# Kernel tuning notes

Hardware: AMD Instinct MI355X
Metric: run time of the kernel (lower is better)

Reference implementation:

```python
import jax, jax.numpy as jnp
import numpy as np

BATCH, SEQ = 2, 2048
HID = 2048          # hidden_size
INTER = 4096        # intermediate_size
STATE = 16          # ssm_state_size
RANK = 128          # time_step_rank
K = 4               # conv_kernel


def setup_inputs() -> dict:
    key = jax.random.key(0)
    ks = jax.random.split(key, 8)
    s = 0.02
    return {
        "hidden_states": jax.random.normal(ks[0], (BATCH, SEQ, HID), jnp.float32),
        "in_proj_w": jax.random.normal(ks[1], (2 * INTER, HID), jnp.float32) * s,
        "conv_w": jax.random.normal(ks[2], (INTER, 1, K), jnp.float32) * s,   # depthwise (O, I/g=1, K)
        "conv_b": jnp.zeros((INTER,), jnp.float32),
        "x_proj_w": jax.random.normal(ks[3], (RANK + 2 * STATE, INTER), jnp.float32) * s,
        "dt_proj_w": jax.random.normal(ks[4], (INTER, RANK), jnp.float32) * s,
        "dt_proj_b": jax.random.normal(ks[5], (INTER,), jnp.float32) * s,
        "A_log": jnp.log(jnp.broadcast_to(jnp.arange(1, STATE + 1, dtype=jnp.float32), (INTER, STATE))),
        "D": jnp.ones((INTER,), jnp.float32),
        "out_proj_w": jax.random.normal(ks[6], (HID, INTER), jnp.float32) * s,
    }


def reference(hidden_states, in_proj_w, conv_w, conv_b, x_proj_w,
              dt_proj_w, dt_proj_b, A_log, D, out_proj_w):
    B, L, _ = hidden_states.shape
    # in_proj -> (B, L, 2*INTER), split into u (SSM input) and gate
    proj = jnp.einsum('blh,ph->blp', hidden_states, in_proj_w)
    u, gate = jnp.split(proj, 2, axis=-1)                       # (B, L, INTER) each
    # depthwise causal conv1d on channel-major layout (B, INTER, L)
    uc = jnp.swapaxes(u, 1, 2)
    conv = jax.lax.conv_general_dilated(
        uc, conv_w, window_strides=(1,), padding=[(K - 1, 0)],
        dimension_numbers=('NCH', 'OIH', 'NCH'), feature_group_count=INTER)
    u = jax.nn.silu(conv + conv_b[None, :, None])               # (B, INTER, L)
    # x_proj: dt-rank + B + C, computed in fp32 like the original
    ssm_p = jnp.einsum('bdl,pd->blp', u, x_proj_w).astype(jnp.float32)
    dt_r, Bm, Cm = jnp.split(ssm_p, [RANK, RANK + STATE], axis=-1)  # (B,L,RANK),(B,L,N),(B,L,N)
    dt = jax.nn.softplus(jnp.einsum('blr,dr->bld', dt_r, dt_proj_w) + dt_proj_b)  # (B, L, INTER)
    A = -jnp.exp(A_log)                                         # (INTER, STATE)

    def step(state, xs):
        dt_t, B_t, C_t, u_t = xs                                # (B,D),(B,N),(B,N),(B,D)
        dA = jnp.exp(dt_t[:, :, None] * A[None])                # (B, D, N)
        state = dA * state + (dt_t * u_t)[:, :, None] * B_t[:, None, :]
        y = jnp.einsum('bdn,bn->bd', state, C_t)
        return state, y

    xs = (jnp.swapaxes(dt, 0, 1),        # (L, B, D)
          jnp.swapaxes(Bm, 0, 1),        # (L, B, N)
          jnp.swapaxes(Cm, 0, 1),        # (L, B, N)
          jnp.moveaxis(u, 2, 0))         # (L, B, D)
    init = jnp.zeros((B, INTER, STATE), jnp.float32)
    _, ys = jax.lax.scan(step, init, xs)                        # (L, B, D)

    y = jnp.moveaxis(ys, 0, 1) + jnp.swapaxes(u, 1, 2) * D[None, None, :]  # skip connection
    y = y * jax.nn.silu(gate)
    return jnp.einsum('bld,hd->blh', y, out_proj_w)             # (B, L, HID)
```

## Files before the change

kernel.cpp:

```cpp
#include <hip/hip_runtime.h>

typedef unsigned int u32;
typedef unsigned short u16;
typedef float f32x4 __attribute__((ext_vector_type(4)));
typedef float f32x16 __attribute__((ext_vector_type(16)));
typedef u16 us4 __attribute__((ext_vector_type(4)));
typedef u16 us8 __attribute__((ext_vector_type(8)));
typedef __bf16 bf16x8 __attribute__((ext_vector_type(8)));

__device__ __forceinline__ u16 f2bf(float f) {
  u32 u = __builtin_bit_cast(u32, f);
  u += 0x7fffu + ((u >> 16) & 1u);
  return (u16)(u >> 16);
}
__device__ __forceinline__ float bf2f(u16 h) {
  u32 u = ((u32)h) << 16;
  return __builtin_bit_cast(float, u);
}
__device__ __forceinline__ void async16(const void* g, void* l) {
  __builtin_amdgcn_global_load_lds((const __attribute__((address_space(1))) void*)g,
                                   (__attribute__((address_space(3))) void*)l, 16, 0, 0);
}

#define STG(GP, LP, OFF, KOFF)                              \
  {                                                         \
    async16((GP) + (KOFF), (LP) + (OFF));                   \
    async16((GP) + 128L * K + (KOFF), (LP) + (OFF) + 4096); \
  }

#define PHASE4(SET, KS, STAGE_STMT, VMW_STMT)                           \
  {                                                                     \
    const u16* Ap_ = As + (SET) * 16384 + (KS) * 8192;                  \
    const u16* Bp_ = Bs + (SET) * 16384 + (KS) * 8192;                  \
    us8 af[8], bf[4];                                                   \
    _Pragma("unroll") for (int i = 0; i < 8; ++i)                       \
        af[i] = *(const us8*)(Ap_ + ra[i]);                             \
    _Pragma("unroll") for (int i = 0; i < 4; ++i)                       \
        bf[i] = *(const us8*)(Bp_ + rb[i]);                             \
    STAGE_STMT;                                                         \
    VMW_STMT;                                                           \
    __builtin_amdgcn_s_setprio(1);                                      \
    _Pragma("unroll") for (int nf = 0; nf < 4; ++nf)                    \
        _Pragma("unroll") for (int mf = 0; mf < 8; ++mf)                \
            acc[mf][nf] = __builtin_amdgcn_mfma_f32_16x16x32_bf16(      \
                __builtin_bit_cast(bf16x8, af[mf]),                     \
                __builtin_bit_cast(bf16x8, bf[nf]), acc[mf][nf],        \
                0, 0, 0);                                               \
    __builtin_amdgcn_s_setprio(0);                                      \
    __builtin_amdgcn_s_barrier();                                       \
  }

__global__ __launch_bounds__(512, 2) void gemm256(const u16* __restrict__ A,
                                                  const u16* __restrict__ B,
                                                  u16* __restrict__ U,
                                                  u16* __restrict__ G, int K) {
  __shared__ __align__(16) u16 As[32768];
  __shared__ __align__(16) u16 Bs[32768];
  const int tid = threadIdx.x;
  const int lane = tid & 63;
  const int wave = tid >> 6;
  const int wm = wave >> 2;
  const int wn = wave & 3;
  const int l15 = lane & 15;
  const int kc2 = lane >> 4;
  const int pc2s = kc2 ^ ((l15 >> 1) & 3);

  const int nbx = (int)gridDim.x;
  const int d = (int)blockIdx.y * nbx + (int)blockIdx.x;
  const int cpn = nbx >> 3;
  const int xcd = d & 7;
  const int s = d >> 3;
  const long colBase = (long)(xcd * cpn + (s % cpn)) << 8;
  const long rowBase = (long)(s / cpn) << 8;

  const int c0 = ((tid & 3) ^ ((tid >> 3) & 3)) << 3;
  const u16* Ag = A + (rowBase + (tid >> 2)) * (long)K + c0;
  const u16* Bg = B + (colBase + (tid >> 2)) * (long)K + c0;
  u16* Alds = As + tid * 8;
  u16* Blds = Bs + tid * 8;

  int ra[8], rb[4];
#pragma unroll
  for (int mf = 0; mf < 8; ++mf)
    ra[mf] = (wm * 128 + mf * 16 + l15) * 32 + pc2s * 8;
#pragma unroll
  for (int nf = 0; nf < 4; ++nf)
    rb[nf] = (wn * 64 + nf * 16 + l15) * 32 + pc2s * 8;

  f32x4 acc[8][4] = {};

  STG(Ag, Alds, 0, 0);
  STG(Bg, Blds, 0, 0);
  STG(Ag, Alds, 8192, 32);
  STG(Bg, Blds, 8192, 32);
  STG(Ag, Alds, 16384, 64);
  STG(Bg, Blds, 16384, 64);
  asm volatile("s_waitcnt vmcnt(8)" ::: "memory");
  __builtin_amdgcn_s_barrier();

  const int nIter = K >> 7;
  for (int t = 0; t < nIter; ++t) {
    const int k1 = (2 * t + 1) * 64;
    const int k2 = (2 * t + 2) * 64;
    const int k3 = (2 * t + 3) * 64;
    const bool full = (t < nIter - 1);
    PHASE4(0, 0,
           {
             STG(Ag, Alds, 24576, k1 + 32);
             STG(Bg, Blds, 24576, k1 + 32);
           },
           { asm volatile("s_waitcnt vmcnt(8)" ::: "memory"); });
    PHASE4(0, 1,
           {
             if (full) {
               STG(Ag, Alds, 0, k2);
               STG(Bg, Blds, 0, k2);
             }
           },
           {
             if (full) asm volatile("s_waitcnt vmcnt(8)" ::: "memory");
             else asm volatile("s_waitcnt vmcnt(4)" ::: "memory");
           });
    PHASE4(1, 0,
           {
             if (full) {
               STG(Ag, Alds, 8192, k2 + 32);
               STG(Bg, Blds, 8192, k2 + 32);
             }
           },
           {
             if (full) asm volatile("s_waitcnt vmcnt(8)" ::: "memory");
             else asm volatile("s_waitcnt vmcnt(0)" ::: "memory");
           });
    PHASE4(1, 1,
           {
             if (full) {
               STG(Ag, Alds, 16384, k3);
               STG(Bg, Blds, 16384, k3);
             }
           },
           { if (full) asm volatile("s_waitcnt vmcnt(8)" ::: "memory"); });
  }

  const int gate = (colBase >= 4096);
  u16* Out = gate ? G : U;
  const long cb = gate ? (colBase - 4096) : colBase;
#pragma unroll
  for (int mf = 0; mf < 8; ++mf) {
    long row0 = rowBase + wm * 128 + mf * 16 + (lane >> 4) * 4;
#pragma unroll
    for (int nf = 0; nf < 4; ++nf) {
      long col = cb + wn * 64 + nf * 16 + l15;
#pragma unroll
      for (int r = 0; r < 4; ++r) {
        float v = acc[mf][nf][r];
        if (gate) v = v / (1.f + __expf(-v));
        Out[(row0 + r) * 4096 + col] = f2bf(v);
      }
    }
  }
}

template <int ACT, bool SPLITK = false>
__global__ __launch_bounds__(256) void gemm_bt(const u16* __restrict__ A,
                                               const u16* __restrict__ B,
                                               void* __restrict__ Cv,
                                               const float* __restrict__ bias,
                                               int K, int ldc) {
  __shared__ __align__(16) u16 As[128 * 64];
  __shared__ __align__(16) u16 Bs[128 * 64];
  const int tid = threadIdx.x;
  const int lane = tid & 63;
  const int wave = tid >> 6;
  const int ln = lane & 31;
  const int hw = lane >> 5;
  const int wm = (wave >> 1) << 6;
  const int wn = (wave & 1) << 6;
  const long rowBase = (long)blockIdx.y << 7;
  const long colBase = (long)blockIdx.x << 7;

  int kStart = 0, kEnd = K;
  if constexpr (SPLITK) {
    int kn = K / gridDim.z;
    kStart = blockIdx.z * kn;
    kEnd = kStart + kn;
  }

  const int rr = tid >> 3;
  const int qg = (tid & 7) ^ (rr & 7);
  const u16* Ag = A + (rowBase + rr) * (long)K + qg * 8;
  const u16* Bg = B + (colBase + rr) * (long)K + qg * 8;
  u16* Al = As + tid * 8;
  u16* Bl = Bs + tid * 8;

  f32x16 acc[2][2] = {};
  const int l7 = ln & 7;

  for (int k0 = kStart; k0 < kEnd; k0 += 64) {
#pragma unroll
    for (int c = 0; c < 4; ++c) {
      async16(Ag + 32L * c * K + k0, Al + 2048 * c);
      async16(Bg + 32L * c * K + k0, Bl + 2048 * c);
    }
    __syncthreads();
#pragma unroll
    for (int s = 0; s < 4; ++s) {
      const int xa = ((s * 2 + hw) ^ l7) * 8;
      us8 af[2], bfr[2];
#pragma unroll
      for (int i = 0; i < 2; ++i)
        af[i] = *(const us8*)(As + (wm + i * 32 + ln) * 64 + xa);
#pragma unroll
      for (int i = 0; i < 2; ++i)
        bfr[i] = *(const us8*)(Bs + (wn + i * 32 + ln) * 64 + xa);
#pragma unroll
      for (int i = 0; i < 2; ++i)
#pragma unroll
        for (int j = 0; j < 2; ++j)
          acc[i][j] = __builtin_amdgcn_mfma_f32_32x32x16_bf16(
              __builtin_bit_cast(bf16x8, af[i]), __builtin_bit_cast(bf16x8, bfr[j]),
              acc[i][j], 0, 0, 0);
    }
    __syncthreads();
  }

  float* Cf = (float*)Cv;
  if constexpr (SPLITK)
    Cf += (size_t)blockIdx.z * ((size_t)gridDim.y * 128 * ldc);

#pragma unroll
  for (int i = 0; i < 2; ++i)
#pragma unroll
    for (int j = 0; j < 2; ++j)
#pragma unroll
      for (int r = 0; r < 16; ++r) {
        long row = rowBase + wm + i * 32 + (r & 3) + 8 * (r >> 2) + 4 * hw;
        long col = colBase + wn + j * 32 + ln;
        float v = acc[i][j][r];
        if constexpr (ACT == 0) {
          Cf[row * ldc + col] = v;
        } else if constexpr (ACT == 3) {
          v += bias[col];
          float sp = (v > 20.f) ? v : log1pf(__expf(v));
          Cf[row * ldc + col] = sp;
        } else if constexpr (ACT == 4) {
          v += bias[col];
          float sp = (v > 20.f) ? v : log1pf(__expf(v));
          ((u16*)Cv)[row * ldc + col] = f2bf(sp);
        }
      }
}

__device__ __forceinline__ void cvt8(const float* __restrict__ in,
                                     u16* __restrict__ out, int i) {
  f32x4 v0 = ((const f32x4*)in)[i * 2];
  f32x4 v1 = ((const f32x4*)in)[i * 2 + 1];
  us8 o;
  o[0] = f2bf(v0[0]); o[1] = f2bf(v0[1]); o[2] = f2bf(v0[2]); o[3] = f2bf(v0[3]);
  o[4] = f2bf(v1[0]); o[5] = f2bf(v1[1]); o[6] = f2bf(v1[2]); o[7] = f2bf(v1[3]);
  ((us8*)out)[i] = o;
}
__global__ __launch_bounds__(256) void cvt_all(
    const float* __restrict__ hs, const float* __restrict__ wIn,
    const float* __restrict__ wOut, const float* __restrict__ wDt,
    const float* __restrict__ wX, u16* __restrict__ Xb, u16* __restrict__ Winb,
    u16* __restrict__ Wob, u16* __restrict__ Wdtb, u16* __restrict__ Wxb) {
  int i = blockIdx.x * 256 + threadIdx.x;
  if (i < 1048576) { cvt8(hs, Xb, i); return; }
  i -= 1048576;
  if (i < 2097152) { cvt8(wIn, Winb, i); return; }
  i -= 2097152;
  if (i < 1048576) { cvt8(wOut, Wob, i); return; }
  i -= 1048576;
  if (i < 65536) { cvt8(wDt, Wdtb, i); return; }
  i -= 65536;
  if (i >= 131072) return;
  int row = (i << 3) >> 12;
  us8 o;
  if (row < 160) {
    f32x4 v0 = ((const f32x4*)wX)[i * 2];
    f32x4 v1 = ((const f32x4*)wX)[i * 2 + 1];
    o[0] = f2bf(v0[0]); o[1] = f2bf(v0[1]); o[2] = f2bf(v0[2]); o[3] = f2bf(v0[3]);
    o[4] = f2bf(v1[0]); o[5] = f2bf(v1[1]); o[6] = f2bf(v1[2]); o[7] = f2bf(v1[3]);
  } else {
    o[0] = 0; o[1] = 0; o[2] = 0; o[3] = 0;
    o[4] = 0; o[5] = 0; o[6] = 0; o[7] = 0;
  }
  ((us8*)Wxb)[i] = o;
}

__global__ __launch_bounds__(256) void xp_reduce(const float* __restrict__ part,
                                                 float* __restrict__ smp,
                                                 u16* __restrict__ dtrb) {
  int i = blockIdx.x * 256 + threadIdx.x;
  const f32x4* p = (const f32x4*)part;
  f32x4 v = p[i];
  v += p[i + 262144];
  v += p[i + 524288];
  v += p[i + 786432];
  ((f32x4*)smp)[i] = v;
  int e = i << 2;
  int c = e & 255;
  if (c < 128) {
    int t = e >> 8;
    us4 o;
    o[0] = f2bf(v[0]); o[1] = f2bf(v[1]); o[2] = f2bf(v[2]); o[3] = f2bf(v[3]);
    *(us4*)(dtrb + t * 128 + c) = o;
  }
}

__global__ __launch_bounds__(256) void conv_silu(const u16* __restrict__ U,
                                                 const float* __restrict__ cw,
                                                 const float* __restrict__ cb,
                                                 u16* __restrict__ out) {
  int i = blockIdx.x * 256 + threadIdx.x;
  int t = i >> 10;
  int d4 = (i & 1023) << 2;
  int l = t & 2047;
  float w[4][4];
#pragma unroll
  for (int j = 0; j < 4; ++j) {
    f32x4 wv = *(const f32x4*)(cw + (d4 + j) * 4);
    w[j][0] = wv[0]; w[j][1] = wv[1]; w[j][2] = wv[2]; w[j][3] = wv[3];
  }
  float r[4] = {cb[d4], cb[d4 + 1], cb[d4 + 2], cb[d4 + 3]};
#pragma unroll
  for (int k = 0; k < 4; ++k) {
    int ll = l - 3 + k;
    if (ll >= 0) {
      us4 xv = *(const us4*)(U + (size_t)(t - 3 + k) * 4096 + d4);
      r[0] += w[0][k] * bf2f(xv[0]);
      r[1] += w[1][k] * bf2f(xv[1]);
      r[2] += w[2][k] * bf2f(xv[2]);
      r[3] += w[3][k] * bf2f(xv[3]);
    }
  }
  us4 o;
#pragma unroll
  for (int j = 0; j < 4; ++j) {
    float v = r[j];
    float s = v / (1.f + __expf(-v));
    o[j] = f2bf(s);
  }
  *(us4*)(out + (size_t)t * 4096 + d4) = o;
}

__global__ __launch_bounds__(256) void scan_part(
    const u16* __restrict__ dt, const u16* __restrict__ ub,
    const float* __restrict__ ssmp, const float* __restrict__ Alog,
    float* __restrict__ Sout, float* __restrict__ dtsumo) {
  const int tid = threadIdx.x;
  const int chunk = blockIdx.x, dgrp = blockIdx.y, b = blockIdx.z;
  const int d = (dgrp << 8) + tid;
  float A[16];
#pragma unroll
  for (int q = 0; q < 4; ++q) {
    f32x4 v = *(const f32x4*)(Alog + d * 16 + q * 4);
    A[q * 4 + 0] = -__expf(v[0]);
    A[q * 4 + 1] = -__expf(v[1]);
    A[q * 4 + 2] = -__expf(v[2]);
    A[q * 4 + 3] = -__expf(v[3]);
  }
  bool fastl = true;
#pragma unroll
  for (int n = 1; n < 16; ++n)
    fastl = fastl && (fabsf(A[n] - (n + 1) * A[0]) <= 1e-4f * (float)(n + 1));
  const bool fast = (__ballot(fastl) == ~0ull);

  const int base = b * 2048 + chunk * 64;
  const u16* dtp = dt + (size_t)base * 4096 + d;
  const u16* up = ub + (size_t)base * 4096 + d;
  const float* Bp = ssmp + (size_t)base * 256 + 128;

  float s[16] = {};
  float dtsum = 0.f;
  float cdt[8], cu[8], ndt[8] = {}, nu[8] = {};
#pragma unroll
  for (int j = 0; j < 8; ++j) {
    cdt[j] = bf2f(dtp[j * 4096]);
    cu[j] = bf2f(up[j * 4096]);
  }
  for (int l0 = 0; l0 < 64; l0 += 8) {
    if (l0 + 8 < 64) {
      int o = (l0 + 8) * 4096;
#pragma unroll
      for (int j = 0; j < 8; ++j) {
        ndt[j] = bf2f(dtp[o + j * 4096]);
        nu[j] = bf2f(up[o + j * 4096]);
      }
    }
    if (fast) {
#pragma unroll
      for (int j = 0; j < 8; ++j) {
        float e1 = __expf(cdt[j] * A[0]);
        float x = cdt[j] * cu[j];
        const float* Bl = Bp + (l0 + j) * 256;
        f32x4 B0 = *(const f32x4*)(Bl);
        f32x4 B1 = *(const f32x4*)(Bl + 4);
        f32x4 B2 = *(const f32x4*)(Bl + 8);
        f32x4 B3 = *(const f32x4*)(Bl + 12);
        float p = 1.f;
#pragma unroll
        for (int n = 0; n < 16; ++n) {
          p *= e1;
          float Bn = (n < 4) ? B0[n & 3] : (n < 8) ? B1[n & 3] : (n < 12) ? B2[n & 3] : B3[n & 3];
          s[n] = fmaf(p, s[n], x * Bn);
        }
        dtsum += cdt[j];
      }
    } else {
#pragma unroll
      for (int j = 0; j < 8; ++j) {
        float x = cdt[j] * cu[j];
        const float* Bl = Bp + (l0 + j) * 256;
        f32x4 B0 = *(const f32x4*)(Bl);
        f32x4 B1 = *(const f32x4*)(Bl + 4);
        f32x4 B2 = *(const f32x4*)(Bl + 8);
        f32x4 B3 = *(const f32x4*)(Bl + 12);
#pragma unroll
        for (int n = 0; n < 16; ++n) {
          float e = __expf(cdt[j] * A[n]);
          float Bn = (n < 4) ? B0[n & 3] : (n < 8) ? B1[n & 3] : (n < 12) ? B2[n & 3] : B3[n & 3];
          s[n] = fmaf(e, s[n], x * Bn);
        }
        dtsum += cdt[j];
      }
    }
#pragma unroll
    for (int j = 0; j < 8; ++j) { cdt[j] = ndt[j]; cu[j] = nu[j]; }
  }
  size_t o = ((size_t)(b * 32 + chunk) * 16) * 4096 + d;
#pragma unroll
  for (int n = 0; n < 16; ++n) Sout[o + (size_t)n * 4096] = s[n];
  dtsumo[(size_t)(b * 32 + chunk) * 4096 + d] = dtsum;
}

__global__ __launch_bounds__(256) void scan_fold(float* S,
                                                 const float* __restrict__ dtsum,
                                                 const float* __restrict__ Alog) {
  const int tid = threadIdx.x;
  const int n = blockIdx.x, dgrp = blockIdx.y, b = blockIdx.z;
  const int d = (dgrp << 8) + tid;
  const float A = -__expf(Alog[d * 16 + n]);
  float run = 0.f;
  for (int c = 0; c < 32; ++c) {
    size_t o = ((size_t)(b * 32 + c) * 16 + n) * 4096 + d;
    float sv = S[o];
    S[o] = run;
    float P = __expf(dtsum[(size_t)(b * 32 + c) * 4096 + d] * A);
    run = fmaf(P, run, sv);
  }
}

__global__ __launch_bounds__(256) void scan_y(
    const u16* __restrict__ dt, const u16* __restrict__ ub,
    const float* __restrict__ ssmp, const u16* __restrict__ gs,
    const float* __restrict__ Alog, const float* __restrict__ Dv,
    const float* __restrict__ Sinit, u16* __restrict__ yb) {
  const int tid = threadIdx.x;
  const int chunk = blockIdx.x, dgrp = blockIdx.y, b = blockIdx.z;
  const int d = (dgrp << 8) + tid;
  float A[16];
#pragma unroll
  for (int q = 0; q < 4; ++q) {
    f32x4 v = *(const f32x4*)(Alog + d * 16 + q * 4);
    A[q * 4 + 0] = -__expf(v[0]);
    A[q * 4 + 1] = -__expf(v[1]);
    A[q * 4 + 2] = -__expf(v[2]);
    A[q * 4 + 3] = -__expf(v[3]);
  }
  bool fastl = true;
#pragma unroll
  for (int n = 1; n < 16; ++n)
    fastl = fastl && (fabsf(A[n] - (n + 1) * A[0]) <= 1e-4f * (float)(n + 1));
  const bool fast = (__ballot(fastl) == ~0ull);
  const float Dd = Dv[d];

  const int base = b * 2048 + chunk * 64;
  const u16* dtp = dt + (size_t)base * 4096 + d;
  const u16* up = ub + (size_t)base * 4096 + d;
  const u16* gp = gs + (size_t)base * 4096 + d;
  const float* Bp = ssmp + (size_t)base * 256 + 128;
  u16* yo = yb + (size_t)base * 4096 + d;

  float s[16];
  {
    size_t o = ((size_t)(b * 32 + chunk) * 16) * 4096 + d;
#pragma unroll
    for (int n = 0; n < 16; ++n) s[n] = Sinit[o + (size_t)n * 4096];
  }

  float cdt[8], cu[8], cg[8], ndt[8] = {}, nu[8] = {}, ng[8] = {};
#pragma unroll
  for (int j = 0; j < 8; ++j) {
    cdt[j] = bf2f(dtp[j * 4096]);
    cu[j] = bf2f(up[j * 4096]);
    cg[j] = bf2f(gp[j * 4096]);
  }
  for (int l0 = 0; l0 < 64; l0 += 8) {
    if (l0 + 8 < 64) {
      int o = (l0 + 8) * 4096;
#pragma unroll
      for (int j = 0; j < 8; ++j) {
        ndt[j] = bf2f(dtp[o + j * 4096]);
        nu[j] = bf2f(up[o + j * 4096]);
        ng[j] = bf2f(gp[o + j * 4096]);
      }
    }
    if (fast) {
#pragma unroll
      for (int j = 0; j < 8; ++j) {
        float e1 = __expf(cdt[j] * A[0]);
        float x = cdt[j] * cu[j];
        const float* Bl = Bp + (l0 + j) * 256;
        f32x4 B0 = *(const f32x4*)(Bl);
        f32x4 B1 = *(const f32x4*)(Bl + 4);
        f32x4 B2 = *(const f32x4*)(Bl + 8);
        f32x4 B3 = *(const f32x4*)(Bl + 12);
        f32x4 C0 = *(const f32x4*)(Bl + 16);
        f32x4 C1 = *(const f32x4*)(Bl + 20);
        f32x4 C2 = *(const f32x4*)(Bl + 24);
        f32x4 C3 = *(const f32x4*)(Bl + 28);
        float p = 1.f;
        float y0 = 0.f, y1 = 0.f, y2 = 0.f, y3 = 0.f;
#pragma unroll
        for (int n = 0; n < 16; ++n) {
          p *= e1;
          float Bn = (n < 4) ? B0[n & 3] : (n < 8) ? B1[n & 3] : (n < 12) ? B2[n & 3] : B3[n & 3];
          float Cn = (n < 4) ? C0[n & 3] : (n < 8) ? C1[n & 3] : (n < 12) ? C2[n & 3] : C3[n & 3];
          s[n] = fmaf(p, s[n], x * Bn);
          if (n < 4) y0 = fmaf(s[n], Cn, y0);
          else if (n < 8) y1 = fmaf(s[n], Cn, y1);
          else if (n < 12) y2 = fmaf(s[n], Cn, y2);
          else y3 = fmaf(s[n], Cn, y3);
        }
        float y = (y0 + y1) + (y2 + y3);
        yo[(l0 + j) * 4096] = f2bf((y + cu[j] * Dd) * cg[j]);
      }
    } else {
#pragma unroll
      for (int j = 0; j < 8; ++j) {
        float x = cdt[j] * cu[j];
        const float* Bl = Bp + (l0 + j) * 256;
        f32x4 B0 = *(const f32x4*)(Bl);
        f32x4 B1 = *(const f32x4*)(Bl + 4);
        f32x4 B2 = *(const f32x4*)(Bl + 8);
        f32x4 B3 = *(const f32x4*)(Bl + 12);
        f32x4 C0 = *(const f32x4*)(Bl + 16);
        f32x4 C1 = *(const f32x4*)(Bl + 20);
        f32x4 C2 = *(const f32x4*)(Bl + 24);
        f32x4 C3 = *(const f32x4*)(Bl + 28);
        float y0 = 0.f, y1 = 0.f, y2 = 0.f, y3 = 0.f;
#pragma unroll
        for (int n = 0; n < 16; ++n) {
          float e = __expf(cdt[j] * A[n]);
          float Bn = (n < 4) ? B0[n & 3] : (n < 8) ? B1[n & 3] : (n < 12) ? B2[n & 3] : B3[n & 3];
          float Cn = (n < 4) ? C0[n & 3] : (n < 8) ? C1[n & 3] : (n < 12) ? C2[n & 3] : C3[n & 3];
          s[n] = fmaf(e, s[n], x * Bn);
          if (n < 4) y0 = fmaf(s[n], Cn, y0);
          else if (n < 8) y1 = fmaf(s[n], Cn, y1);
          else if (n < 12) y2 = fmaf(s[n], Cn, y2);
          else y3 = fmaf(s[n], Cn, y3);
        }
        float y = (y0 + y1) + (y2 + y3);
        yo[(l0 + j) * 4096] = f2bf((y + cu[j] * Dd) * cg[j]);
      }
    }
#pragma unroll
    for (int j = 0; j < 8; ++j) { cdt[j] = ndt[j]; cu[j] = nu[j]; cg[j] = ng[j]; }
  }
}

extern "C" void kernel_launch(void* const* d_in, const int* in_sizes, int n_in,
                              void* d_out, int out_size, void* d_ws,
                              size_t ws_size, hipStream_t stream) {
  (void)in_sizes; (void)n_in; (void)out_size; (void)ws_size;
  const float* hs = (const float*)d_in[0];
  const float* wIn = (const float*)d_in[1];
  const float* cw = (const float*)d_in[2];
  const float* cb = (const float*)d_in[3];
  const float* wX = (const float*)d_in[4];
  const float* wDt = (const float*)d_in[5];
  const float* bDt = (const float*)d_in[6];
  const float* Alog = (const float*)d_in[7];
  const float* Dv = (const float*)d_in[8];
  const float* wOut = (const float*)d_in[9];

  const size_t MB = 1ull << 20;
  char* w = (char*)d_ws;
  u16* Xb = (u16*)(w + 0 * MB);
  u16* Winb = (u16*)(w + 16 * MB);
  u16* Pu = (u16*)(w + 48 * MB);
  u16* Dtb = (u16*)(w + 0 * MB);
  u16* Yb = (u16*)(w + 64 * MB);
  u16* Ub = (u16*)(w + 96 * MB);
  u16* Wxb = (u16*)(w + 128 * MB);
  float* Smp = (float*)(w + 130 * MB);
  u16* Dtrb = (u16*)(w + 134 * MB);
  u16* Wdtb = (u16*)(w + 135 * MB);
  u16* Wob = (u16*)(w + 136 * MB);
  float* Schk = (float*)(w + 152 * MB);
  float* Xpart = (float*)(w + 152 * MB);
  float* Dtsum = (float*)(w + 168 * MB);
  u16* Pg = (u16*)d_out;

  cvt_all<<<17152, 256, 0, stream>>>(hs, wIn, wOut, wDt, wX, Xb, Winb, Wob, Wdtb, Wxb);
  gemm256<<<dim3(32, 16), 512, 0, stream>>>(Xb, Winb, Pu, Pg, 2048);
  conv_silu<<<16384, 256, 0, stream>>>(Pu, cw, cb, Ub);
  gemm_bt<0, true><<<dim3(2, 32, 4), 256, 0, stream>>>(Ub, Wxb, Xpart, nullptr, 4096, 256);
  xp_reduce<<<1024, 256, 0, stream>>>(Xpart, Smp, Dtrb);
  gemm_bt<4><<<dim3(32, 32), 256, 0, stream>>>(Dtrb, Wdtb, Dtb, bDt, 128, 4096);
  scan_part<<<dim3(32, 16, 2), 256, 0, stream>>>(Dtb, Ub, Smp, Alog, Schk, Dtsum);
  scan_fold<<<dim3(16, 16, 2), 256, 0, stream>>>(Schk, Dtsum, Alog);
  scan_y<<<dim3(32, 16, 2), 256, 0, stream>>>(Dtb, Ub, Smp, Pg, Alog, Dv, Schk, Yb);
  gemm_bt<0><<<dim3(16, 32), 256, 0, stream>>>(Yb, Wob, (float*)d_out, nullptr, 4096, 2048);
}
```

Before: 627.8 us.

## Shrink in_proj GEMM LDS pipeline from four to two stages

```diff
diff --git a/kernel.cpp b/kernel.cpp
--- a/kernel.cpp
+++ b/kernel.cpp
@@ -28,17 +28,15 @@
     async16((GP) + 128L * K + (KOFF), (LP) + (OFF) + 4096); \
   }
 
-#define PHASE4(SET, KS, STAGE_STMT, VMW_STMT)                           \
+#define PHASE2(SLOT, QK2, FULL, LAST62)                                 \
   {                                                                     \
-    const u16* Ap_ = As + (SET) * 16384 + (KS) * 8192;                  \
-    const u16* Bp_ = Bs + (SET) * 16384 + (KS) * 8192;                  \
+    const u16* Ap_ = As + (SLOT) * 8192;                                \
+    const u16* Bp_ = Bs + (SLOT) * 8192;                                \
     us8 af[8], bf[4];                                                   \
     _Pragma("unroll") for (int i = 0; i < 8; ++i)                       \
         af[i] = *(const us8*)(Ap_ + ra[i]);                             \
     _Pragma("unroll") for (int i = 0; i < 4; ++i)                       \
         bf[i] = *(const us8*)(Bp_ + rb[i]);                             \
-    STAGE_STMT;                                                         \
-    VMW_STMT;                                                           \
     __builtin_amdgcn_s_setprio(1);                                      \
     _Pragma("unroll") for (int nf = 0; nf < 4; ++nf)                    \
         _Pragma("unroll") for (int mf = 0; mf < 8; ++mf)                \
@@ -48,14 +46,24 @@
                 0, 0, 0);                                               \
     __builtin_amdgcn_s_setprio(0);                                      \
     __builtin_amdgcn_s_barrier();                                       \
+    if (FULL) {                                                         \
+      STG(Ag, Alds, (SLOT) * 8192, (QK2));                              \
+      STG(Bg, Blds, (SLOT) * 8192, (QK2));                              \
+    }                                                                   \
+    if (FULL) {                                                         \
+      asm volatile("s_waitcnt vmcnt(4)" ::: "memory");                  \
+    } else if (LAST62) {                                                \
+      asm volatile("s_waitcnt vmcnt(0)" ::: "memory");                  \
+    }                                                                   \
+    __builtin_amdgcn_s_barrier();                                       \
   }
 
 __global__ __launch_bounds__(512, 2) void gemm256(const u16* __restrict__ A,
                                                   const u16* __restrict__ B,
                                                   u16* __restrict__ U,
                                                   u16* __restrict__ G, int K) {
-  __shared__ __align__(16) u16 As[32768];
-  __shared__ __align__(16) u16 Bs[32768];
+  __shared__ __align__(16) u16 As[16384];
+  __shared__ __align__(16) u16 Bs[16384];
   const int tid = threadIdx.x;
   const int lane = tid & 63;
   const int wave = tid >> 6;
@@ -93,53 +101,15 @@
   STG(Bg, Blds, 0, 0);
   STG(Ag, Alds, 8192, 32);
   STG(Bg, Blds, 8192, 32);
-  STG(Ag, Alds, 16384, 64);
-  STG(Bg, Blds, 16384, 64);
-  asm volatile("s_waitcnt vmcnt(8)" ::: "memory");
+  asm volatile("s_waitcnt vmcnt(4)" ::: "memory");
   __builtin_amdgcn_s_barrier();
 
-  const int nIter = K >> 7;
-  for (int t = 0; t < nIter; ++t) {
-    const int k1 = (2 * t + 1) * 64;
-    const int k2 = (2 * t + 2) * 64;
-    const int k3 = (2 * t + 3) * 64;
-    const bool full = (t < nIter - 1);
-    PHASE4(0, 0,
-           {
-             STG(Ag, Alds, 24576, k1 + 32);
-             STG(Bg, Blds, 24576, k1 + 32);
-           },
-           { asm volatile("s_waitcnt vmcnt(8)" ::: "memory"); });
-    PHASE4(0, 1,
-           {
-             if (full) {
-               STG(Ag, Alds, 0, k2);
-               STG(Bg, Blds, 0, k2);
-             }
-           },
-           {
-             if (full) asm volatile("s_waitcnt vmcnt(8)" ::: "memory");
-             else asm volatile("s_waitcnt vmcnt(4)" ::: "memory");
-           });
-    PHASE4(1, 0,
-           {
-             if (full) {
-               STG(Ag, Alds, 8192, k2 + 32);
-               STG(Bg, Blds, 8192, k2 + 32);
-             }
-           },
-           {
-             if (full) asm volatile("s_waitcnt vmcnt(8)" ::: "memory");
-             else asm volatile("s_waitcnt vmcnt(0)" ::: "memory");
-           });
-    PHASE4(1, 1,
-           {
-             if (full) {
-               STG(Ag, Alds, 16384, k3);
-               STG(Bg, Blds, 16384, k3);
-             }
-           },
-           { if (full) asm volatile("s_waitcnt vmcnt(8)" ::: "memory"); });
+  const int nQ = K >> 5;
+  for (int t = 0; t < nQ; t += 2) {
+    const bool f0 = (t + 2) < nQ;
+    const bool f1 = (t + 3) < nQ;
+    PHASE2(0, (t + 2) * 32, f0, !f0);
+    PHASE2(1, (t + 3) * 32, f1, false);
   }
 
   const int gate = (colBase >= 4096);
```

Result: no change. 626.4 us (-0.2%).
